# Kernel optimization log

Hardware: AMD Instinct MI355X
Metric: run time of the kernel (lower is better)

Reference implementation:

```python
import jax, jax.numpy as jnp
import numpy as np

N, E, B, D, H, L = 50000, 800000, 16, 64, 128, 2


def _lin(h, w, b):
    return h @ w + b


def _scatter_mean(v, idx, n):
    s = jax.ops.segment_sum(v, idx, num_segments=n)
    c = jax.ops.segment_sum(jnp.ones((v.shape[0],), v.dtype), idx, num_segments=n)
    return s / jnp.maximum(c, 1.0)[:, None]


def setup_inputs() -> dict:
    key = jax.random.key(0)
    ks = iter(jax.random.split(key, 40))

    def p(*shape):
        return jax.random.normal(next(ks), shape, dtype=jnp.float32) * 0.05

    inp = {
        "x": jax.random.normal(next(ks), (N, D), dtype=jnp.float32),
        "edge_attr": jax.random.normal(next(ks), (E, D), dtype=jnp.float32),
        "u": jax.random.normal(next(ks), (B, D), dtype=jnp.float32),
        "e_w1": p(L, 4 * D, H), "e_b1": p(L, H),
        "e_w2": p(L, H, H), "e_b2": p(L, H),
        "e_w3": p(L, H, D), "e_b3": p(L, D),
        "n1_w1": p(L, 2 * D, H), "n1_b1": p(L, H),
        "n1_w2": p(L, H, H), "n1_b2": p(L, H),
        "n2_w1": p(L, D + H + D, H), "n2_b1": p(L, H),
        "n2_w2": p(L, H, D), "n2_b2": p(L, D),
        "g_w1": p(L, 3 * D, H), "g_b1": p(L, H),
        "g_w2": p(L, H, D), "g_b2": p(L, D),
        "edge_index": jax.random.randint(next(ks), (2, E), 0, N, dtype=jnp.int32),
        "batch": jnp.sort(jax.random.randint(next(ks), (N,), 0, B, dtype=jnp.int32)),
    }
    return inp


def _forward(x, edge_attr, u, params, edge_index, batch):
    row, col = edge_index[0], edge_index[1]
    eb = batch[row]  # [E] graph id per edge
    x0, e0, u0 = x, edge_attr, u
    for l in range(L):
        (e_w1, e_b1, e_w2, e_b2, e_w3, e_b3,
         n1_w1, n1_b1, n1_w2, n1_b2,
         n2_w1, n2_b1, n2_w2, n2_b2,
         g_w1, g_b1, g_w2, g_b2) = [pm[l] for pm in params]
        # Edge model: [E, e+2n+u] -> MLP -> [E, D]
        h = jnp.concatenate([x[row], x[col], edge_attr, u[eb]], axis=1)
        h = jax.nn.relu(_lin(h, e_w1, e_b1))
        h = jax.nn.relu(_lin(h, e_w2, e_b2))
        edge_attr = _lin(h, e_w3, e_b3)
        # Node model: gather src node + edge, MLP1, scatter_mean onto dest, MLP2
        se = jnp.concatenate([x[row], edge_attr], axis=1)  # [E, 2D]
        se = _lin(jax.nn.relu(_lin(se, n1_w1, n1_b1)), n1_w2, n1_b2)
        agg = _scatter_mean(se, col, N)  # [N, H]
        xh = jnp.concatenate([x, agg, u[batch]], axis=1)
        x = _lin(jax.nn.relu(_lin(xh, n2_w1, n2_b1)), n2_w2, n2_b2)
        # Global model: per-graph means of updated nodes/edges
        e_agg = _scatter_mean(edge_attr, eb, B)
        n_agg = _scatter_mean(x, batch, B)
        uh = jnp.concatenate([u, n_agg, e_agg], axis=1)
        u = _lin(jax.nn.relu(_lin(uh, g_w1, g_b1)), g_w2, g_b2)
    return x + x0, edge_attr + e0, u + u0


def reference(x, edge_attr, u, e_w1, e_b1, e_w2, e_b2, e_w3, e_b3, n1_w1, n1_b1, n1_w2, n1_b2, n2_w1, n2_b1, n2_w2, n2_b2, g_w1, g_b1, g_w2, g_b2, edge_index, batch):
    params = (e_w1, e_b1, e_w2, e_b2, e_w3, e_b3,
              n1_w1, n1_b1, n1_w2, n1_b2,
              n2_w1, n2_b1, n2_w2, n2_b2,
              g_w1, g_b1, g_w2, g_b2)
    return _forward(x, edge_attr, u, params, edge_index, batch)
```

## Files before the change

kernel.cpp:

```cpp
#include <hip/hip_runtime.h>

#define N_NODES 50000
#define E_EDGES 800000
#define NG 16
#define DD 64
#define HH 128
#define NB_SCAN 49
#define EREP 32

typedef __attribute__((ext_vector_type(8))) __bf16 bf16x8;
typedef __attribute__((ext_vector_type(4))) float f32x4;
typedef unsigned int uint;
typedef unsigned short ushort;
typedef __attribute__((ext_vector_type(4))) uint uint4v;

#define MFMA16(a,b,c) __builtin_amdgcn_mfma_f32_16x16x32_bf16((a),(b),(c),0,0,0)

__device__ __forceinline__ ushort f2bf(float f){
  uint u = __builtin_bit_cast(uint, f);
  u += 0x7fffu + ((u >> 16) & 1u);
  return (ushort)(u >> 16);
}
__device__ __forceinline__ uint pk2(float a, float b){
  return (uint)f2bf(a) | ((uint)f2bf(b) << 16);
}
__device__ __forceinline__ float bflo(uint u){ return __builtin_bit_cast(float, u << 16); }
__device__ __forceinline__ float bfhi(uint u){ return __builtin_bit_cast(float, u & 0xffff0000u); }

__device__ __forceinline__ void bar(){
  asm volatile("s_waitcnt lgkmcnt(0)" ::: "memory");
  __builtin_amdgcn_s_barrier();
}
#define VMWAIT(n) asm volatile("s_waitcnt vmcnt(" #n ")" ::: "memory")

__device__ __forceinline__ void gload16(const void* g, void* l){
  __builtin_amdgcn_global_load_lds(
      (const __attribute__((address_space(1))) unsigned int*)g,
      (__attribute__((address_space(3))) unsigned int*)l, 16, 0, 0);
}

__device__ __forceinline__ bf16x8 ldfrag(const char* base, int row, int byteoff){
  uint4v v = *(const uint4v*)(base + row*256 + (byteoff ^ ((row & 7) << 4)));
  return __builtin_bit_cast(bf16x8, v);
}
__device__ __forceinline__ uint4v ld_chunk(const char* base, int row, int c16){
  return *(const uint4v*)(base + row*256 + ((c16*16) ^ ((row & 7) << 4)));
}
__device__ __forceinline__ void st_h(char* base, int row, int col, float v){
  *(ushort*)(base + row*256 + ((col*2) ^ ((row & 7) << 4))) = f2bf(v);
}
__device__ __forceinline__ void st_chunk(char* base, int row, int c16, uint4v v){
  *(uint4v*)(base + row*256 + ((c16*16) ^ ((row & 7) << 4))) = v;
}
__device__ __forceinline__ bf16x8 ldfrag128(const char* base, int row, int byteoff){
  uint4v v = *(const uint4v*)(base + row*128 + (byteoff ^ ((row & 7) << 4)));
  return __builtin_bit_cast(bf16x8, v);
}
__device__ __forceinline__ void st_chunk128(char* base, int row, int c16, uint4v v){
  *(uint4v*)(base + row*128 + ((c16*16) ^ ((row & 7) << 4))) = v;
}
__device__ __forceinline__ void pack16_128(char* dst, int r, int c16, const float* src){
  float4 lo = *(const float4*)src;
  float4 hi = *(const float4*)(src + 4);
  uint4v v; v.x = pk2(lo.x, lo.y); v.y = pk2(lo.z, lo.w);
  v.z = pk2(hi.x, hi.y); v.w = pk2(hi.z, hi.w);
  st_chunk128(dst, r, c16, v);
}

__device__ __forceinline__ void stage_b(char* sB, const ushort* wt,
                                        int Nout, int Ktot, int koff, int t, int stride){
  for (int task = t; task < Nout*16; task += stride){
    int n = task >> 4, c = task & 15;
    uint4v v = *(const uint4v*)(wt + (long)n*Ktot + koff + c*8);
    st_chunk(sB, n, c, v);
  }
}
template<int NT>
__device__ __forceinline__ void gemm_acc(const char* A, const char* B,
                                         int wv, int l15, int lhi, f32x4* acc){
  #pragma unroll
  for (int kt = 0; kt < 4; ++kt){
    bf16x8 a = ldfrag(A, wv*16 + l15, kt*64 + lhi*16);
    #pragma unroll
    for (int n = 0; n < NT; ++n){
      bf16x8 bb = ldfrag(B, n*16 + l15, kt*64 + lhi*16);
      acc[n] = MFMA16(a, bb, acc[n]);
    }
  }
}
template<int NT, bool RELU>
__device__ __forceinline__ void epi_lds(char* dst, const f32x4* acc, const float* bias,
                                        int wv, int l15, int lhi){
  #pragma unroll
  for (int n = 0; n < NT; ++n){
    float bv = bias[n*16 + l15];
    #pragma unroll
    for (int j = 0; j < 4; ++j){
      int r = wv*16 + lhi*4 + j;
      float v = acc[n][j] + bv;
      if (RELU) v = fmaxf(v, 0.f);
      st_h(dst, r, n*16 + l15, v);
    }
  }
}

__global__ void convert_x(const float* __restrict__ x, ushort* __restrict__ xbf){
  int i = blockIdx.x*256 + threadIdx.x;
  if (i < (N_NODES*DD)/8){
    float4 lo = *(const float4*)(x + (long)i*8);
    float4 hi = *(const float4*)(x + (long)i*8 + 4);
    uint4v v; v.x = pk2(lo.x, lo.y); v.y = pk2(lo.z, lo.w);
    v.z = pk2(hi.x, hi.y); v.w = pk2(hi.z, hi.w);
    *(uint4v*)(xbf + (long)i*8) = v;
  }
}

__global__ void pack_weights(const float* __restrict__ e1, const float* __restrict__ e2,
                             const float* __restrict__ e3, const float* __restrict__ n12,
                             const float* __restrict__ n21, const float* __restrict__ n22,
                             ushort* __restrict__ out){
  int idx = blockIdx.x * 256 + threadIdx.x;
  int l = idx / 114688, r = idx % 114688;
  const float* src; int K, N, off;
  if      (r <  32768){ src = e1;  K = 256; N = 128; off = 0; }
  else if (r <  49152){ src = e2;  K = 128; N = 128; off = 32768; }
  else if (r <  57344){ src = e3;  K = 128; N = 64;  off = 49152; }
  else if (r <  73728){ src = n12; K = 128; N = 128; off = 57344; }
  else if (r < 106496){ src = n21; K = 256; N = 128; off = 73728; }
  else                { src = n22; K = 128; N = 64;  off = 106496; }
  int q = r - off; int k = q / N; int n = q % N;
  out[(long)l*139264 + off + n*K + k] = f2bf(src[(long)l*K*N + q]);
}

__global__ void make_wc(const float* __restrict__ n1w1, const float* __restrict__ ew3,
                        const float* __restrict__ n1b1, const float* __restrict__ eb3,
                        ushort* __restrict__ packed, float* __restrict__ biasc){
  int l = blockIdx.x, t = threadIdx.x;
  const float* W1 = n1w1 + (long)l*128*128;
  const float* W3 = ew3 + (long)l*128*64;
  ushort* wc = packed + (long)l*139264 + 114688;
  for (int i = t; i < 8192; i += 256){
    int k = i >> 7, n = i & 127;
    wc[n*192 + k] = f2bf(W1[k*128 + n]);
  }
  for (int i = t; i < 16384; i += 256){
    int k2 = i >> 7, n = i & 127;
    float s = 0.f;
    for (int m = 0; m < 64; ++m) s += W3[k2*64 + m] * W1[(64 + m)*128 + n];
    wc[n*192 + 64 + k2] = f2bf(s);
  }
  if (t < 128){
    float s = n1b1[l*128 + t];
    for (int m = 0; m < 64; ++m) s += eb3[l*64 + m] * W1[(64 + m)*128 + t];
    biasc[l*128 + t] = s;
  }
}

__global__ void hist_kernel(const int* __restrict__ edge_index, const int* __restrict__ batch,
                            int* __restrict__ deg, float* __restrict__ cnt_eb){
  __shared__ float h[NG];
  int t = threadIdx.x;
  if (t < NG) h[t] = 0.f;
  __syncthreads();
  int e = blockIdx.x * 256 + t;
  if (e < E_EDGES){
    atomicAdd(deg + edge_index[E_EDGES + e], 1);
    atomicAdd(&h[batch[edge_index[e]]], 1.f);
  }
  __syncthreads();
  if (t < NG) atomicAdd(cnt_eb + t, h[t]);
}
__global__ void count_nodes_kernel(const int* __restrict__ batch, float* __restrict__ cnt_b){
  __shared__ float h[NG];
  int t = threadIdx.x;
  if (t < NG) h[t] = 0.f;
  __syncthreads();
  int n = blockIdx.x * 256 + t;
  if (n < N_NODES) atomicAdd(&h[batch[n]], 1.f);
  __syncthreads();
  if (t < NG) atomicAdd(cnt_b + t, h[t]);
}
__global__ void scan_a(const int* __restrict__ deg, int* __restrict__ bsum){
  __shared__ int red[1024];
  int i = blockIdx.x*1024 + threadIdx.x;
  red[threadIdx.x] = (i < N_NODES) ? deg[i] : 0;
  __syncthreads();
  for (int s = 512; s > 0; s >>= 1){
    if ((int)threadIdx.x < s) red[threadIdx.x] += red[threadIdx.x + s];
    __syncthreads();
  }
  if (threadIdx.x == 0) bsum[blockIdx.x] = red[0];
}
__global__ void scan_b(const int* __restrict__ bsum, int* __restrict__ bbase){
  if (threadIdx.x == 0){
    int run = 0;
    for (int b = 0; b < NB_SCAN; ++b){ int v = bsum[b]; bbase[b] = run; run += v; }
  }
}
__global__ void scan_c(const int* __restrict__ deg, const int* __restrict__ bbase,
                       int* __restrict__ off, int* __restrict__ cursor){
  __shared__ int sc[1024];
  int i = blockIdx.x*1024 + threadIdx.x;
  int v = (i < N_NODES) ? deg[i] : 0;
  sc[threadIdx.x] = v;
  __syncthreads();
  for (int d = 1; d < 1024; d <<= 1){
    int add = ((int)threadIdx.x >= d) ? sc[threadIdx.x - d] : 0;
    __syncthreads();
    sc[threadIdx.x] += add;
    __syncthreads();
  }
  if (i < N_NODES){
    int ex = sc[threadIdx.x] - v + bbase[blockIdx.x];
    off[i] = ex; cursor[i] = ex;
  }
}
__global__ void fill_kernel(const int* __restrict__ edge_index, int* __restrict__ cursor,
                            int* __restrict__ pos){
  int e = blockIdx.x*256 + threadIdx.x;
  if (e < E_EDGES){
    int c = edge_index[E_EDGES + e];
    pos[e] = atomicAdd(&cursor[c], 1);
  }
}

__global__ __launch_bounds__(256, 3) void k123_kernel(
    const ushort* __restrict__ xbf, const float* e_cur,
    const float* __restrict__ u_cur,
    const int* __restrict__ ei, const int* __restrict__ batch,
    const ushort* __restrict__ w1t, const ushort* __restrict__ w2t,
    const float* __restrict__ be1, const float* __restrict__ be2,
    ushort* h2g)
{
  __shared__ __align__(16) char lds[49152];
  __shared__ int sRow[128], sCol[128], sEb[128];
  char* A  = lds;
  char* B  = lds + 16384;
  char* OV = lds + 16384;
  const int t = threadIdx.x;
  const int wv = t >> 6, l15 = t & 15, lhi = (t >> 4) & 3;
  const int ebase = blockIdx.x * 128;

  if (t < 128){
    int r = ei[ebase + t];
    sRow[t] = r; sCol[t] = ei[E_EDGES + ebase + t]; sEb[t] = batch[r];
  }
  __syncthreads();

  f32x4 acc[2][8];
  #pragma unroll
  for (int m = 0; m < 2; ++m)
    #pragma unroll
    for (int n = 0; n < 8; ++n) acc[m][n] = f32x4{0,0,0,0};

  for (int c = 0; c < 4; ++c){
    #pragma unroll
    for (int it = 0; it < 4; ++it){
      int task = t + it*256, r = task >> 3, c16 = task & 7;
      if (c == 0)
        st_chunk128(A, r, c16, *(const uint4v*)(xbf + (long)sRow[r]*DD + c16*8));
      else if (c == 1)
        st_chunk128(A, r, c16, *(const uint4v*)(xbf + (long)sCol[r]*DD + c16*8));
      else if (c == 2)
        pack16_128(A, r, c16, e_cur + (long)(ebase + r)*DD + c16*8);
      else
        pack16_128(A, r, c16, u_cur + (long)sEb[r]*DD + c16*8);
    }
    #pragma unroll
    for (int it = 0; it < 4; ++it){
      int task = t + it*256, n = task >> 3, c16 = task & 7;
      st_chunk128(B, n, c16, *(const uint4v*)(w1t + (long)n*256 + c*64 + c16*8));
    }
    __syncthreads();
    #pragma unroll
    for (int kt = 0; kt < 2; ++kt){
      bf16x8 a0 = ldfrag128(A, wv*32 + l15,      kt*64 + lhi*16);
      bf16x8 a1 = ldfrag128(A, wv*32 + 16 + l15, kt*64 + lhi*16);
      #pragma unroll
      for (int n = 0; n < 8; ++n){
        bf16x8 bb = ldfrag128(B, n*16 + l15, kt*64 + lhi*16);
        acc[0][n] = MFMA16(a0, bb, acc[0][n]);
        acc[1][n] = MFMA16(a1, bb, acc[1][n]);
      }
    }
    __syncthreads();
  }
  #pragma unroll
  for (int m = 0; m < 2; ++m)
    #pragma unroll
    for (int n = 0; n < 8; ++n){
      int col = n*16 + l15;
      float bv = be1[col];
      #pragma unroll
      for (int j = 0; j < 4; ++j)
        st_h(OV, wv*32 + m*16 + lhi*4 + j, col, fmaxf(acc[m][n][j] + bv, 0.f));
    }
  __syncthreads();

  #pragma unroll
  for (int m = 0; m < 2; ++m)
    #pragma unroll
    for (int n = 0; n < 8; ++n) acc[m][n] = f32x4{0,0,0,0};
  for (int kc = 0; kc < 2; ++kc){
    #pragma unroll
    for (int it = 0; it < 4; ++it){
      int task = t + it*256, n = task >> 3, c16 = task & 7;
      st_chunk128(A, n, c16, *(const uint4v*)(w2t + (long)n*128 + kc*64 + c16*8));
    }
    __syncthreads();
    #pragma unroll
    for (int kt = 0; kt < 2; ++kt){
      bf16x8 a0 = ldfrag(OV, wv*32 + l15,      kc*128 + kt*64 + lhi*16);
      bf16x8 a1 = ldfrag(OV, wv*32 + 16 + l15, kc*128 + kt*64 + lhi*16);
      #pragma unroll
      for (int n = 0; n < 8; ++n){
        bf16x8 bb = ldfrag128(A, n*16 + l15, kt*64 + lhi*16);
        acc[0][n] = MFMA16(a0, bb, acc[0][n]);
        acc[1][n] = MFMA16(a1, bb, acc[1][n]);
      }
    }
    __syncthreads();
  }
  #pragma unroll
  for (int m = 0; m < 2; ++m)
    #pragma unroll
    for (int n = 0; n < 8; ++n){
      int col = n*16 + l15;
      float bv = be2[col];
      #pragma unroll
      for (int j = 0; j < 4; ++j)
        st_h(OV, wv*32 + m*16 + lhi*4 + j, col, fmaxf(acc[m][n][j] + bv, 0.f));
    }
  __syncthreads();
  #pragma unroll
  for (int it = 0; it < 8; ++it){
    int task = t + it*256, r = task >> 4, c16 = task & 15;
    *(uint4v*)(h2g + (long)(ebase + r)*HH + c16*8) = ld_chunk(OV, r, c16);
  }
}

template<bool CSR>
__global__ __launch_bounds__(256, 2) void k45_kernel(
    const ushort* __restrict__ xbf, const ushort* h2g,
    const int* __restrict__ ei, const int* __restrict__ batch,
    const int* __restrict__ pos_arr,
    const ushort* __restrict__ w3t, const ushort* __restrict__ wct,
    const ushort* __restrict__ w5t,
    const float* __restrict__ be3, const float* __restrict__ biasc,
    const float* __restrict__ bn12,
    float* e_outf, const float* __restrict__ e_resid,
    ushort* __restrict__ se_buf, float* __restrict__ agg_sum,
    float* __restrict__ e_agg_rep, int has_resid)
{
  __shared__ __align__(16) char lds[49152];
  __shared__ float sEagg[NG*DD];
  __shared__ int sRow[128];
  __shared__ int sDst[128];
  char* S0 = lds;
  char* S1 = lds + 16384;
  char* S2 = lds + 32768;
  char* OV = lds;
  const int t = threadIdx.x;
  const int wv = t >> 6, lane = t & 63, l15 = t & 15, lhi = (t >> 4) & 3;
  const int ebase = blockIdx.x * 128;

  auto GL = [&](const ushort* base, long stride, int koff, char* slot){
    #pragma unroll
    for (int it = 0; it < 4; ++it){
      int q = (wv*4 + it)*64 + lane;
      int r = q >> 3, cp = q & 7;
      gload16(base + (long)r*stride + koff + ((cp ^ (r & 7))*8),
              slot + (wv*4 + it)*1024);
    }
  };

  if (t < 128){
    int r = ei[ebase + t];
    sDst[t] = CSR ? pos_arr[ebase + t] : ei[E_EDGES + ebase + t];
    sRow[t] = r | (batch[r] << 16);
  }
  GL(wct, 192, 0, S1);
  GL(h2g + (long)ebase*HH, HH, 0, S2);
  bf16x8 b3[4][4];
  #pragma unroll
  for (int n = 0; n < 4; ++n)
    #pragma unroll
    for (int kk = 0; kk < 4; ++kk)
      b3[n][kk] = *(const bf16x8*)(w3t + (long)(n*16 + l15)*128 + kk*32 + lhi*8);
  for (int i = t; i < NG*DD; i += 256) sEagg[i] = 0.f;
  __syncthreads();

  #pragma unroll
  for (int it = 0; it < 4; ++it){
    int task = t + it*256, r = task >> 3, c16 = task & 7;
    st_chunk128(S0, r, c16,
        *(const uint4v*)(xbf + (long)(sRow[r] & 0xffff)*DD + c16*8));
  }
  __syncthreads();

  f32x4 acc4[2][8], acc3[2][4];
  #pragma unroll
  for (int m = 0; m < 2; ++m){
    #pragma unroll
    for (int n = 0; n < 8; ++n) acc4[m][n] = f32x4{0,0,0,0};
    #pragma unroll
    for (int n = 0; n < 4; ++n) acc3[m][n] = f32x4{0,0,0,0};
  }
  auto MM = [&](const char* A, const char* B){
    #pragma unroll
    for (int kt = 0; kt < 2; ++kt){
      bf16x8 a0 = ldfrag128(A, wv*32 + l15,      kt*64 + lhi*16);
      bf16x8 a1 = ldfrag128(A, wv*32 + 16 + l15, kt*64 + lhi*16);
      #pragma unroll
      for (int n = 0; n < 8; ++n){
        bf16x8 bb = ldfrag128(B, n*16 + l15, kt*64 + lhi*16);
        acc4[0][n] = MFMA16(a0, bb, acc4[0][n]);
        acc4[1][n] = MFMA16(a1, bb, acc4[1][n]);
      }
    }
  };
  auto MM3 = [&](const char* A, const char* B, int kkbase){
    #pragma unroll
    for (int kt = 0; kt < 2; ++kt){
      bf16x8 a0 = ldfrag128(A, wv*32 + l15,      kt*64 + lhi*16);
      bf16x8 a1 = ldfrag128(A, wv*32 + 16 + l15, kt*64 + lhi*16);
      #pragma unroll
      for (int n = 0; n < 8; ++n){
        bf16x8 bb = ldfrag128(B, n*16 + l15, kt*64 + lhi*16);
        acc4[0][n] = MFMA16(a0, bb, acc4[0][n]);
        acc4[1][n] = MFMA16(a1, bb, acc4[1][n]);
      }
      #pragma unroll
      for (int n = 0; n < 4; ++n){
        acc3[0][n] = MFMA16(a0, b3[n][kkbase + kt], acc3[0][n]);
        acc3[1][n] = MFMA16(a1, b3[n][kkbase + kt], acc3[1][n]);
      }
    }
  };

  MM(S0, S1);
  bar();
  GL(wct, 192, 64, S1);
  GL(h2g + (long)ebase*HH, HH, 64, S0);
  VMWAIT(4);
  __builtin_amdgcn_s_barrier();
  MM3(S2, S1, 0);
  bar();
  GL(wct, 192, 128, S1);
  GL(w5t, 128, 0, S2);
  VMWAIT(4);
  __builtin_amdgcn_s_barrier();
  MM3(S0, S1, 2);
  bar();
  #pragma unroll
  for (int m = 0; m < 2; ++m)
    #pragma unroll
    for (int n = 0; n < 8; ++n){
      int col = n*16 + l15;
      float bv = biasc[col];
      #pragma unroll
      for (int j = 0; j < 4; ++j)
        st_h(OV, wv*32 + m*16 + lhi*4 + j, col, fmaxf(acc4[m][n][j] + bv, 0.f));
    }
  VMWAIT(0);
  bar();
  f32x4 acc5[2][8];
  #pragma unroll
  for (int m = 0; m < 2; ++m)
    #pragma unroll
    for (int n = 0; n < 8; ++n) acc5[m][n] = f32x4{0,0,0,0};
  #pragma unroll
  for (int kt = 0; kt < 2; ++kt){
    bf16x8 a0 = ldfrag(OV, wv*32 + l15,      kt*64 + lhi*16);
    bf16x8 a1 = ldfrag(OV, wv*32 + 16 + l15, kt*64 + lhi*16);
    #pragma unroll
    for (int n = 0; n < 8; ++n){
      bf16x8 bb = ldfrag128(S2, n*16 + l15, kt*64 + lhi*16);
      acc5[0][n] = MFMA16(a0, bb, acc5[0][n]);
      acc5[1][n] = MFMA16(a1, bb, acc5[1][n]);
    }
  }
  bar();
  GL(w5t, 128, 64, S2);
  VMWAIT(0);
  __builtin_amdgcn_s_barrier();
  #pragma unroll
  for (int kt = 0; kt < 2; ++kt){
    bf16x8 a0 = ldfrag(OV, wv*32 + l15,      128 + kt*64 + lhi*16);
    bf16x8 a1 = ldfrag(OV, wv*32 + 16 + l15, 128 + kt*64 + lhi*16);
    #pragma unroll
    for (int n = 0; n < 8; ++n){
      bf16x8 bb = ldfrag128(S2, n*16 + l15, kt*64 + lhi*16);
      acc5[0][n] = MFMA16(a0, bb, acc5[0][n]);
      acc5[1][n] = MFMA16(a1, bb, acc5[1][n]);
    }
  }
  bar();

  if (CSR){
    #pragma unroll
    for (int m = 0; m < 2; ++m)
      #pragma unroll
      for (int n = 0; n < 8; ++n){
        int col = n*16 + l15;
        float bv = bn12[col];
        #pragma unroll
        for (int j = 0; j < 4; ++j)
          st_h(OV, wv*32 + m*16 + lhi*4 + j, col, acc5[m][n][j] + bv);
      }
    bar();
    #pragma unroll
    for (int it = 0; it < 8; ++it){
      int task = t + it*256, r = task >> 4, c16 = task & 15;
      *(uint4v*)(se_buf + (long)sDst[r]*HH + c16*8) = ld_chunk(OV, r, c16);
    }
  } else {
    #pragma unroll
    for (int m = 0; m < 2; ++m)
      #pragma unroll
      for (int n = 0; n < 8; ++n){
        int col = n*16 + l15;
        float bv = bn12[col];
        #pragma unroll
        for (int j = 0; j < 4; ++j){
          int row = wv*32 + m*16 + lhi*4 + j;
          atomicAdd(agg_sum + (long)sDst[row]*HH + col, acc5[m][n][j] + bv);
        }
      }
  }
  #pragma unroll
  for (int m = 0; m < 2; ++m)
    #pragma unroll
    for (int n = 0; n < 4; ++n){
      int col = n*16 + l15;
      float bv = be3[col];
      #pragma unroll
      for (int j = 0; j < 4; ++j){
        int row = wv*32 + m*16 + lhi*4 + j;
        float v = acc3[m][n][j] + bv;
        long eg = (long)(ebase + row)*DD + col;
        e_outf[eg] = has_resid ? (v + e_resid[eg]) : v;
        atomicAdd(&sEagg[(sRow[row] >> 16)*DD + col], v);
      }
    }
  __syncthreads();
  float* dst = e_agg_rep + (long)(blockIdx.x & (EREP - 1))*NG*DD;
  for (int i = t; i < NG*DD; i += 256) atomicAdd(dst + i, sEagg[i]);
}

template<bool CSR>
__global__ __launch_bounds__(256, 2) void node_kernel(
    const float* __restrict__ x_cur, const float* __restrict__ u_cur,
    const float* __restrict__ x_resid, const int* __restrict__ batch,
    const ushort* __restrict__ se_buf, const int* __restrict__ deg,
    const int* __restrict__ off, const float* __restrict__ agg_sum,
    const ushort* __restrict__ w_n21, const ushort* __restrict__ w_n22,
    const float* __restrict__ b_n21, const float* __restrict__ b_n22,
    float* __restrict__ x_out, float* __restrict__ n_agg, int has_resid)
{
  __shared__ __align__(16) char sA[16384];
  __shared__ __align__(16) char sB[32768];
  __shared__ __align__(16) char sH[16384];
  __shared__ int sBat[64], sDeg[64], sOff[64];
  __shared__ float sRinv[64];
  __shared__ float sNagg[NG*DD];

  const int t = threadIdx.x;
  const int wv = t >> 6, ln = t & 63, l15 = ln & 15, lhi = ln >> 4;
  const int n0 = blockIdx.x * 64;

  if (t < 64){
    int nd = n0 + t;
    int ok = nd < N_NODES;
    sBat[t] = ok ? batch[nd] : 0;
    int d = ok ? deg[nd] : 0;
    sDeg[t] = d;
    sOff[t] = ok ? off[nd] : 0;
    sRinv[t] = 1.f / fmaxf((float)d, 1.f);
  }
  for (int i = t; i < NG*DD; i += 256) sNagg[i] = 0.f;
  __syncthreads();

  float s[32];
  const int r4 = t >> 2, q = t & 3;
  if (CSR){
    #pragma unroll
    for (int k = 0; k < 32; ++k) s[k] = 0.f;
    int d = sDeg[r4], o = sOff[r4];
    for (int i = 0; i < d; ++i){
      const ushort* src = se_buf + (long)(o + i)*HH + q*32;
      #pragma unroll
      for (int c = 0; c < 4; ++c){
        uint4v v = *(const uint4v*)(src + c*8);
        #pragma unroll
        for (int jj = 0; jj < 4; ++jj){
          s[c*8 + jj*2]     += bflo(v[jj]);
          s[c*8 + jj*2 + 1] += bfhi(v[jj]);
        }
      }
    }
    float riv = sRinv[r4];
    #pragma unroll
    for (int k = 0; k < 32; ++k) s[k] *= riv;
  }

  f32x4 acc[8];
  #pragma unroll
  for (int n = 0; n < 8; ++n) acc[n] = f32x4{0.f,0.f,0.f,0.f};

  for (int half = 0; half < 2; ++half){
    if (CSR){
      for (int task = t; task < 512; task += 256){
        int r = task >> 3, c = task & 7;
        int nd = n0 + r;
        bool ok = nd < N_NODES;
        float4 lo = {0,0,0,0}, hi = {0,0,0,0};
        if (ok){
          const float* src = (half == 0) ? (x_cur + (long)nd*DD + c*8)
                                         : (u_cur + (long)sBat[r]*DD + c*8);
          lo = *(const float4*)src; hi = *(const float4*)(src + 4);
        }
        uint4v v; v.x = pk2(lo.x, lo.y); v.y = pk2(lo.z, lo.w);
        v.z = pk2(hi.x, hi.y); v.w = pk2(hi.z, hi.w);
        st_chunk(sA, r, (half == 0) ? c : (8 + c), v);
      }
      if ((half == 0 && q < 2) || (half == 1 && q >= 2)){
        int cbase = (half == 0) ? (8 + q*4) : ((q - 2)*4);
        #pragma unroll
        for (int cc = 0; cc < 4; ++cc){
          uint4v v;
          v.x = pk2(s[cc*8+0], s[cc*8+1]); v.y = pk2(s[cc*8+2], s[cc*8+3]);
          v.z = pk2(s[cc*8+4], s[cc*8+5]); v.w = pk2(s[cc*8+6], s[cc*8+7]);
          st_chunk(sA, r4, cbase + cc, v);
        }
      }
    } else {
      for (int task = t; task < 1024; task += 256){
        int r = task >> 4, c = task & 15;
        int nd = n0 + r;
        bool ok = nd < N_NODES;
        float scale = 1.f;
        const float* src;
        if (half == 0){
          if (c < 8) src = x_cur + (long)nd*DD + c*8;
          else { src = agg_sum + (long)nd*HH + (c-8)*8; scale = sRinv[r]; }
        } else {
          if (c < 8){ src = agg_sum + (long)nd*HH + 64 + c*8; scale = sRinv[r]; }
          else src = u_cur + (long)sBat[r]*DD + (c-8)*8;
        }
        float4 lo = {0,0,0,0}, hi = {0,0,0,0};
        if (ok){ lo = *(const float4*)src; hi = *(const float4*)(src + 4); }
        uint4v v; v.x = pk2(lo.x*scale, lo.y*scale); v.y = pk2(lo.z*scale, lo.w*scale);
        v.z = pk2(hi.x*scale, hi.y*scale); v.w = pk2(hi.z*scale, hi.w*scale);
        st_chunk(sA, r, c, v);
      }
    }
    stage_b(sB, w_n21, 128, 256, half*128, t, 256);
    __syncthreads();
    gemm_acc<8>(sA, sB, wv, l15, lhi, acc);
    __syncthreads();
  }
  epi_lds<8, true>(sH, acc, b_n21, wv, l15, lhi);
  stage_b(sB, w_n22, 64, 128, 0, t, 256);
  __syncthreads();

  f32x4 acc2[4];
  #pragma unroll
  for (int n = 0; n < 4; ++n) acc2[n] = f32x4{0.f,0.f,0.f,0.f};
  gemm_acc<4>(sH, sB, wv, l15, lhi, acc2);

  #pragma unroll
  for (int n = 0; n < 4; ++n){
    float bv = b_n22[n*16 + l15];
    #pragma unroll
    for (int j = 0; j < 4; ++j){
      int r = wv*16 + lhi*4 + j;
      int nd = n0 + r;
      if (nd < N_NODES){
        int col = n*16 + l15;
        float v = acc2[n][j] + bv;
        long xg = (long)nd*DD + col;
        x_out[xg] = has_resid ? (v + x_resid[xg]) : v;
        atomicAdd(&sNagg[sBat[r]*DD + col], v);
      }
    }
  }
  __syncthreads();
  for (int i = t; i < NG*DD; i += 256) atomicAdd(n_agg + i, sNagg[i]);
}

__global__ void global_kernel(const float* __restrict__ u_cur, const float* __restrict__ n_agg,
                              const float* __restrict__ e_agg_rep, const float* __restrict__ cnt_b,
                              const float* __restrict__ cnt_e,
                              const float* __restrict__ g_w1, const float* __restrict__ g_b1,
                              const float* __restrict__ g_w2, const float* __restrict__ g_b2,
                              const float* __restrict__ u_resid, float* __restrict__ u_out,
                              int has_resid)
{
  int g = blockIdx.x, t = threadIdx.x;
  __shared__ float uh[192];
  __shared__ float hb[128];
  float v;
  if (t < 64)       v = u_cur[g*64 + t];
  else if (t < 128) v = n_agg[g*64 + (t-64)] / fmaxf(cnt_b[g], 1.f);
  else {
    float s = 0.f;
    for (int c = 0; c < EREP; ++c) s += e_agg_rep[c*NG*DD + g*64 + (t-128)];
    v = s / fmaxf(cnt_e[g], 1.f);
  }
  uh[t] = v;
  __syncthreads();
  if (t < 128){
    float s = g_b1[t];
    for (int k = 0; k < 192; ++k) s += uh[k] * g_w1[k*128 + t];
    hb[t] = fmaxf(s, 0.f);
  }
  __syncthreads();
  if (t < 64){
    float s = g_b2[t];
    for (int k = 0; k < 128; ++k) s += hb[k] * g_w2[k*64 + t];
    if (has_resid) s += u_resid[g*64 + t];
    u_out[g*64 + t] = s;
  }
}

extern "C" void kernel_launch(void* const* d_in, const int* in_sizes, int n_in,
                              void* d_out, int out_size, void* d_ws, size_t ws_size,
                              hipStream_t stream)
{
  const float* x0   = (const float*)d_in[0];
  const float* e0   = (const float*)d_in[1];
  const float* u0   = (const float*)d_in[2];
  const float* e_w1 = (const float*)d_in[3];
  const float* e_b1 = (const float*)d_in[4];
  const float* e_w2 = (const float*)d_in[5];
  const float* e_b2 = (const float*)d_in[6];
  const float* e_w3 = (const float*)d_in[7];
  const float* e_b3 = (const float*)d_in[8];
  const float* n1_w1 = (const float*)d_in[9];
  const float* n1_b1 = (const float*)d_in[10];
  const float* n1_w2 = (const float*)d_in[11];
  const float* n1_b2 = (const float*)d_in[12];
  const float* n2_w1 = (const float*)d_in[13];
  const float* n2_b1 = (const float*)d_in[14];
  const float* n2_w2 = (const float*)d_in[15];
  const float* n2_b2 = (const float*)d_in[16];
  const float* g_w1 = (const float*)d_in[17];
  const float* g_b1 = (const float*)d_in[18];
  const float* g_w2 = (const float*)d_in[19];
  const float* g_b2 = (const float*)d_in[20];
  const int* edge_index = (const int*)d_in[21];
  const int* batch      = (const int*)d_in[22];

  float* out_x = (float*)d_out;
  float* out_e = out_x + (long)N_NODES*DD;
  float* out_u = out_e + (long)E_EDGES*DD;

  char* ws = (char*)d_ws;
  int*   deg    = (int*)(ws + 0);
  int*   off    = (int*)(ws + 200000);
  int*   cursor = (int*)(ws + 400000);
  int*   bsum   = (int*)(ws + 600000);
  int*   bbase  = (int*)(ws + 600256);
  float* cnt_eb = (float*)(ws + 600512);
  float* cnt_b  = (float*)(ws + 600576);
  float* n_agg  = (float*)(ws + 604736);
  float* biascf = (float*)(ws + 608832);
  ushort* packed = (ushort*)(ws + 609856);
  float* e_agg_rep = (float*)(ws + 1166912);
  ushort* xbf = (ushort*)(ws + 1297984);
  const size_t big = 7697984;
  bool use_csr = ws_size >= (size_t)(big + 204800000 + 3200000);
  ushort* se_buf = (ushort*)(ws + big);
  int*    pos    = (int*)(ws + big + 204800000);
  float*  agg_sum = (float*)(ws + big);

  (void)hipMemsetAsync(deg, 0, 200000, stream);
  (void)hipMemsetAsync(cnt_eb, 0, 128, stream);
  pack_weights<<<896, 256, 0, stream>>>(e_w1, e_w2, e_w3, n1_w2, n2_w1, n2_w2, packed);
  make_wc<<<2, 256, 0, stream>>>(n1_w1, e_w3, n1_b1, e_b3, packed, biascf);
  hist_kernel<<<3125, 256, 0, stream>>>(edge_index, batch, deg, cnt_eb);
  count_nodes_kernel<<<196, 256, 0, stream>>>(batch, cnt_b);
  if (use_csr){
    scan_a<<<NB_SCAN, 1024, 0, stream>>>(deg, bsum);
    scan_b<<<1, 64, 0, stream>>>(bsum, bbase);
    scan_c<<<NB_SCAN, 1024, 0, stream>>>(deg, bbase, off, cursor);
    fill_kernel<<<3125, 256, 0, stream>>>(edge_index, cursor, pos);
  }

  const float* xc = x0;
  const float* ec = e0;
  const float* uc = u0;
  for (int l = 0; l < 2; ++l){
    (void)hipMemsetAsync(n_agg, 0, 4096, stream);
    (void)hipMemsetAsync(e_agg_rep, 0, EREP*NG*DD*4, stream);
    if (!use_csr)
      (void)hipMemsetAsync(agg_sum, 0, (size_t)N_NODES*HH*4, stream);
    convert_x<<<1563, 256, 0, stream>>>(xc, xbf);
    const ushort* P = packed + (long)l*139264;
    k123_kernel<<<6250, 256, 0, stream>>>(
        xbf, ec, uc, edge_index, batch,
        P + 0, P + 32768, e_b1 + l*128, e_b2 + l*128,
        (ushort*)out_e);
    if (use_csr){
      k45_kernel<true><<<6250, 256, 0, stream>>>(
          xbf, (const ushort*)out_e, edge_index, batch, pos,
          P + 49152, P + 114688, P + 57344,
          e_b3 + l*64, biascf + l*128, n1_b2 + l*128,
          out_e, e0, se_buf, agg_sum, e_agg_rep, l == 1);
      node_kernel<true><<<782, 256, 0, stream>>>(
          xc, uc, x0, batch, se_buf, deg, off, agg_sum,
          P + 73728, P + 106496, n2_b1 + l*128, n2_b2 + l*64,
          out_x, n_agg, l == 1);
    } else {
      k45_kernel<false><<<6250, 256, 0, stream>>>(
          xbf, (const ushort*)out_e, edge_index, batch, pos,
          P + 49152, P + 114688, P + 57344,
          e_b3 + l*64, biascf + l*128, n1_b2 + l*128,
          out_e, e0, se_buf, agg_sum, e_agg_rep, l == 1);
      node_kernel<false><<<782, 256, 0, stream>>>(
          xc, uc, x0, batch, se_buf, deg, off, agg_sum,
          P + 73728, P + 106496, n2_b1 + l*128, n2_b2 + l*64,
          out_x, n_agg, l == 1);
    }
    global_kernel<<<NG, 192, 0, stream>>>(
        uc, n_agg, e_agg_rep, cnt_b, cnt_eb,
        g_w1 + l*192*128, g_b1 + l*128, g_w2 + l*128*64, g_b2 + l*64,
        u0, out_u, l == 1);
    xc = out_x; ec = out_e; uc = out_u;
  }
}
```

Baseline: 1.758 ms.

## Fuse edge MLP and node-MLP1 into one kernel with 64-edge tiles

Merges the separate edge-MLP (k123) and node-message (k45) kernels into a single edge_fused kernel that processes 64 edges per block. The intermediate h2 no longer makes a round trip through global memory, and weights are staged through double-buffered LDS slots. Layer-0 edge output is written as bf16 for the layer-1 read, and node_kernel emits bf16 x directly so the per-layer convert_x launch is removed on the CSR path. The trade-offs are more LDS per block (about 72KB), lower occupancy, and re-staging all weights for every 64-edge tile. The async global_load_lds path is also replaced with plain synchronous loads.

```diff
diff --git a/kernel.cpp b/kernel.cpp
--- a/kernel.cpp
+++ b/kernel.cpp
@@ -31,13 +31,6 @@
   asm volatile("s_waitcnt lgkmcnt(0)" ::: "memory");
   __builtin_amdgcn_s_barrier();
 }
-#define VMWAIT(n) asm volatile("s_waitcnt vmcnt(" #n ")" ::: "memory")
-
-__device__ __forceinline__ void gload16(const void* g, void* l){
-  __builtin_amdgcn_global_load_lds(
-      (const __attribute__((address_space(1))) unsigned int*)g,
-      (__attribute__((address_space(3))) unsigned int*)l, 16, 0, 0);
-}
 
 __device__ __forceinline__ bf16x8 ldfrag(const char* base, int row, int byteoff){
   uint4v v = *(const uint4v*)(base + row*256 + (byteoff ^ ((row & 7) << 4)));
@@ -56,8 +49,14 @@
   uint4v v = *(const uint4v*)(base + row*128 + (byteoff ^ ((row & 7) << 4)));
   return __builtin_bit_cast(bf16x8, v);
 }
+__device__ __forceinline__ uint4v ld_chunk128(const char* base, int row, int c16){
+  return *(const uint4v*)(base + row*128 + ((c16*16) ^ ((row & 7) << 4)));
+}
 __device__ __forceinline__ void st_chunk128(char* base, int row, int c16, uint4v v){
   *(uint4v*)(base + row*128 + ((c16*16) ^ ((row & 7) << 4))) = v;
+}
+__device__ __forceinline__ void st_h128(char* base, int row, int col, float v){
+  *(ushort*)(base + row*128 + ((col*2) ^ ((row & 7) << 4))) = f2bf(v);
 }
 __device__ __forceinline__ void pack16_128(char* dst, int r, int c16, const float* src){
   float4 lo = *(const float4*)src;
@@ -224,163 +223,54 @@
   }
 }
 
-__global__ __launch_bounds__(256, 3) void k123_kernel(
-    const ushort* __restrict__ xbf, const float* e_cur,
+template<bool CSR, bool EBF>
+__global__ __launch_bounds__(256, 2) void edge_fused(
+    const ushort* __restrict__ xbf, const float* e_f32, const ushort* e_bf,
     const float* __restrict__ u_cur,
     const int* __restrict__ ei, const int* __restrict__ batch,
+    const int* __restrict__ pos_arr,
     const ushort* __restrict__ w1t, const ushort* __restrict__ w2t,
-    const float* __restrict__ be1, const float* __restrict__ be2,
-    ushort* h2g)
-{
-  __shared__ __align__(16) char lds[49152];
-  __shared__ int sRow[128], sCol[128], sEb[128];
-  char* A  = lds;
-  char* B  = lds + 16384;
-  char* OV = lds + 16384;
-  const int t = threadIdx.x;
-  const int wv = t >> 6, l15 = t & 15, lhi = (t >> 4) & 3;
-  const int ebase = blockIdx.x * 128;
-
-  if (t < 128){
-    int r = ei[ebase + t];
-    sRow[t] = r; sCol[t] = ei[E_EDGES + ebase + t]; sEb[t] = batch[r];
-  }
-  __syncthreads();
-
-  f32x4 acc[2][8];
-  #pragma unroll
-  for (int m = 0; m < 2; ++m)
-    #pragma unroll
-    for (int n = 0; n < 8; ++n) acc[m][n] = f32x4{0,0,0,0};
-
-  for (int c = 0; c < 4; ++c){
-    #pragma unroll
-    for (int it = 0; it < 4; ++it){
-      int task = t + it*256, r = task >> 3, c16 = task & 7;
-      if (c == 0)
-        st_chunk128(A, r, c16, *(const uint4v*)(xbf + (long)sRow[r]*DD + c16*8));
-      else if (c == 1)
-        st_chunk128(A, r, c16, *(const uint4v*)(xbf + (long)sCol[r]*DD + c16*8));
-      else if (c == 2)
-        pack16_128(A, r, c16, e_cur + (long)(ebase + r)*DD + c16*8);
-      else
-        pack16_128(A, r, c16, u_cur + (long)sEb[r]*DD + c16*8);
-    }
-    #pragma unroll
-    for (int it = 0; it < 4; ++it){
-      int task = t + it*256, n = task >> 3, c16 = task & 7;
-      st_chunk128(B, n, c16, *(const uint4v*)(w1t + (long)n*256 + c*64 + c16*8));
-    }
-    __syncthreads();
-    #pragma unroll
-    for (int kt = 0; kt < 2; ++kt){
-      bf16x8 a0 = ldfrag128(A, wv*32 + l15,      kt*64 + lhi*16);
-      bf16x8 a1 = ldfrag128(A, wv*32 + 16 + l15, kt*64 + lhi*16);
-      #pragma unroll
-      for (int n = 0; n < 8; ++n){
-        bf16x8 bb = ldfrag128(B, n*16 + l15, kt*64 + lhi*16);
-        acc[0][n] = MFMA16(a0, bb, acc[0][n]);
-        acc[1][n] = MFMA16(a1, bb, acc[1][n]);
-      }
-    }
-    __syncthreads();
-  }
-  #pragma unroll
-  for (int m = 0; m < 2; ++m)
-    #pragma unroll
-    for (int n = 0; n < 8; ++n){
-      int col = n*16 + l15;
-      float bv = be1[col];
-      #pragma unroll
-      for (int j = 0; j < 4; ++j)
-        st_h(OV, wv*32 + m*16 + lhi*4 + j, col, fmaxf(acc[m][n][j] + bv, 0.f));
-    }
-  __syncthreads();
-
-  #pragma unroll
-  for (int m = 0; m < 2; ++m)
-    #pragma unroll
-    for (int n = 0; n < 8; ++n) acc[m][n] = f32x4{0,0,0,0};
-  for (int kc = 0; kc < 2; ++kc){
-    #pragma unroll
-    for (int it = 0; it < 4; ++it){
-      int task = t + it*256, n = task >> 3, c16 = task & 7;
-      st_chunk128(A, n, c16, *(const uint4v*)(w2t + (long)n*128 + kc*64 + c16*8));
-    }
-    __syncthreads();
-    #pragma unroll
-    for (int kt = 0; kt < 2; ++kt){
-      bf16x8 a0 = ldfrag(OV, wv*32 + l15,      kc*128 + kt*64 + lhi*16);
-      bf16x8 a1 = ldfrag(OV, wv*32 + 16 + l15, kc*128 + kt*64 + lhi*16);
-      #pragma unroll
-      for (int n = 0; n < 8; ++n){
-        bf16x8 bb = ldfrag128(A, n*16 + l15, kt*64 + lhi*16);
-        acc[0][n] = MFMA16(a0, bb, acc[0][n]);
-        acc[1][n] = MFMA16(a1, bb, acc[1][n]);
-      }
-    }
-    __syncthreads();
-  }
-  #pragma unroll
-  for (int m = 0; m < 2; ++m)
-    #pragma unroll
-    for (int n = 0; n < 8; ++n){
-      int col = n*16 + l15;
-      float bv = be2[col];
-      #pragma unroll
-      for (int j = 0; j < 4; ++j)
-        st_h(OV, wv*32 + m*16 + lhi*4 + j, col, fmaxf(acc[m][n][j] + bv, 0.f));
-    }
-  __syncthreads();
-  #pragma unroll
-  for (int it = 0; it < 8; ++it){
-    int task = t + it*256, r = task >> 4, c16 = task & 15;
-    *(uint4v*)(h2g + (long)(ebase + r)*HH + c16*8) = ld_chunk(OV, r, c16);
-  }
-}
-
-template<bool CSR>
-__global__ __launch_bounds__(256, 2) void k45_kernel(
-    const ushort* __restrict__ xbf, const ushort* h2g,
-    const int* __restrict__ ei, const int* __restrict__ batch,
-    const int* __restrict__ pos_arr,
     const ushort* __restrict__ w3t, const ushort* __restrict__ wct,
     const ushort* __restrict__ w5t,
+    const float* __restrict__ be1, const float* __restrict__ be2,
     const float* __restrict__ be3, const float* __restrict__ biasc,
     const float* __restrict__ bn12,
     float* e_outf, const float* __restrict__ e_resid,
     ushort* __restrict__ se_buf, float* __restrict__ agg_sum,
     float* __restrict__ e_agg_rep, int has_resid)
 {
-  __shared__ __align__(16) char lds[49152];
+  __shared__ __align__(16) char lds[73728];
   __shared__ float sEagg[NG*DD];
-  __shared__ int sRow[128];
-  __shared__ int sDst[128];
-  char* S0 = lds;
-  char* S1 = lds + 16384;
-  char* S2 = lds + 32768;
-  char* OV = lds;
+  __shared__ int sRow[64];
+  __shared__ int sCol[64];
+  __shared__ int sDst[64];
+  char* X  = lds;
+  char* A0 = lds + 8192;
+  char* A1 = lds + 16384;
+  char* W0 = lds + 24576;
+  char* W1 = lds + 40960;
+  char* OV = lds + 57344;
   const int t = threadIdx.x;
-  const int wv = t >> 6, lane = t & 63, l15 = t & 15, lhi = (t >> 4) & 3;
-  const int ebase = blockIdx.x * 128;
-
-  auto GL = [&](const ushort* base, long stride, int koff, char* slot){
+  const int wv = t >> 6, l15 = t & 15, lhi = (t >> 4) & 3;
+  const int ebase = blockIdx.x * 64;
+
+  auto WSTAGE = [&](char* W, const ushort* wt, int K, int coff){
     #pragma unroll
     for (int it = 0; it < 4; ++it){
-      int q = (wv*4 + it)*64 + lane;
-      int r = q >> 3, cp = q & 7;
-      gload16(base + (long)r*stride + koff + ((cp ^ (r & 7))*8),
-              slot + (wv*4 + it)*1024);
+      int task = t + it*256, n = task >> 3, c16 = task & 7;
+      st_chunk128(W, n, c16, *(const uint4v*)(wt + (long)n*K + coff + c16*8));
     }
   };
 
-  if (t < 128){
+  if (t < 64){
     int r = ei[ebase + t];
-    sDst[t] = CSR ? pos_arr[ebase + t] : ei[E_EDGES + ebase + t];
+    int c = ei[E_EDGES + ebase + t];
     sRow[t] = r | (batch[r] << 16);
-  }
-  GL(wct, 192, 0, S1);
-  GL(h2g + (long)ebase*HH, HH, 0, S2);
+    sCol[t] = c;
+    sDst[t] = CSR ? pos_arr[ebase + t] : c;
+  }
+  WSTAGE(W0, w1t, 256, 0);
+  WSTAGE(W1, w1t, 256, 64);
   bf16x8 b3[4][4];
   #pragma unroll
   for (int n = 0; n < 4; ++n)
@@ -390,159 +280,220 @@
   for (int i = t; i < NG*DD; i += 256) sEagg[i] = 0.f;
   __syncthreads();
 
-  #pragma unroll
-  for (int it = 0; it < 4; ++it){
+  uint4v xr[2], xc[2], eu[2];
+  float4 ef[4];
+  #pragma unroll
+  for (int it = 0; it < 2; ++it){
     int task = t + it*256, r = task >> 3, c16 = task & 7;
-    st_chunk128(S0, r, c16,
-        *(const uint4v*)(xbf + (long)(sRow[r] & 0xffff)*DD + c16*8));
-  }
-  __syncthreads();
-
-  f32x4 acc4[2][8], acc3[2][4];
-  #pragma unroll
-  for (int m = 0; m < 2; ++m){
-    #pragma unroll
-    for (int n = 0; n < 8; ++n) acc4[m][n] = f32x4{0,0,0,0};
-    #pragma unroll
-    for (int n = 0; n < 4; ++n) acc3[m][n] = f32x4{0,0,0,0};
-  }
-  auto MM = [&](const char* A, const char* B){
+    xr[it] = *(const uint4v*)(xbf + (long)(sRow[r] & 0xffff)*DD + c16*8);
+    xc[it] = *(const uint4v*)(xbf + (long)sCol[r]*DD + c16*8);
+    if (EBF) eu[it] = *(const uint4v*)(e_bf + (long)(ebase + r)*HH + c16*8);
+    else { ef[2*it]   = *(const float4*)(e_f32 + (long)(ebase + r)*DD + c16*8);
+           ef[2*it+1] = *(const float4*)(e_f32 + (long)(ebase + r)*DD + c16*8 + 4); }
+  }
+  #pragma unroll
+  for (int it = 0; it < 2; ++it){
+    int task = t + it*256, r = task >> 3, c16 = task & 7;
+    st_chunk128(X, r, c16, xr[it]);
+  }
+  __syncthreads();
+
+  f32x4 acc1[8];
+  #pragma unroll
+  for (int n = 0; n < 8; ++n) acc1[n] = f32x4{0,0,0,0};
+  auto MM128 = [&](const char* A, const char* W, f32x4* acc){
     #pragma unroll
     for (int kt = 0; kt < 2; ++kt){
-      bf16x8 a0 = ldfrag128(A, wv*32 + l15,      kt*64 + lhi*16);
-      bf16x8 a1 = ldfrag128(A, wv*32 + 16 + l15, kt*64 + lhi*16);
+      bf16x8 a = ldfrag128(A, wv*16 + l15, kt*64 + lhi*16);
       #pragma unroll
       for (int n = 0; n < 8; ++n){
-        bf16x8 bb = ldfrag128(B, n*16 + l15, kt*64 + lhi*16);
-        acc4[0][n] = MFMA16(a0, bb, acc4[0][n]);
-        acc4[1][n] = MFMA16(a1, bb, acc4[1][n]);
+        bf16x8 bb = ldfrag128(W, n*16 + l15, kt*64 + lhi*16);
+        acc[n] = MFMA16(a, bb, acc[n]);
       }
     }
   };
-  auto MM3 = [&](const char* A, const char* B, int kkbase){
+  f32x4 acc3[4];
+  #pragma unroll
+  for (int n = 0; n < 4; ++n) acc3[n] = f32x4{0,0,0,0};
+  auto MMOV = [&](int cbase, const char* W, f32x4* acc){
     #pragma unroll
     for (int kt = 0; kt < 2; ++kt){
-      bf16x8 a0 = ldfrag128(A, wv*32 + l15,      kt*64 + lhi*16);
-      bf16x8 a1 = ldfrag128(A, wv*32 + 16 + l15, kt*64 + lhi*16);
+      bf16x8 a = ldfrag(OV, wv*16 + l15, cbase + kt*64 + lhi*16);
       #pragma unroll
       for (int n = 0; n < 8; ++n){
-        bf16x8 bb = ldfrag128(B, n*16 + l15, kt*64 + lhi*16);
-        acc4[0][n] = MFMA16(a0, bb, acc4[0][n]);
-        acc4[1][n] = MFMA16(a1, bb, acc4[1][n]);
-      }
-      #pragma unroll
-      for (int n = 0; n < 4; ++n){
-        acc3[0][n] = MFMA16(a0, b3[n][kkbase + kt], acc3[0][n]);
-        acc3[1][n] = MFMA16(a1, b3[n][kkbase + kt], acc3[1][n]);
+        bf16x8 bb = ldfrag128(W, n*16 + l15, kt*64 + lhi*16);
+        acc[n] = MFMA16(a, bb, acc[n]);
       }
     }
   };
-
-  MM(S0, S1);
-  bar();
-  GL(wct, 192, 64, S1);
-  GL(h2g + (long)ebase*HH, HH, 64, S0);
-  VMWAIT(4);
-  __builtin_amdgcn_s_barrier();
-  MM3(S2, S1, 0);
-  bar();
-  GL(wct, 192, 128, S1);
-  GL(w5t, 128, 0, S2);
-  VMWAIT(4);
-  __builtin_amdgcn_s_barrier();
-  MM3(S0, S1, 2);
-  bar();
-  #pragma unroll
-  for (int m = 0; m < 2; ++m)
+  auto MMOV3 = [&](int cbase, const char* W, f32x4* acc, int kkb){
+    #pragma unroll
+    for (int kt = 0; kt < 2; ++kt){
+      bf16x8 a = ldfrag(OV, wv*16 + l15, cbase + kt*64 + lhi*16);
+      #pragma unroll
+      for (int n = 0; n < 8; ++n){
+        bf16x8 bb = ldfrag128(W, n*16 + l15, kt*64 + lhi*16);
+        acc[n] = MFMA16(a, bb, acc[n]);
+      }
+      #pragma unroll
+      for (int n = 0; n < 4; ++n)
+        acc3[n] = MFMA16(a, b3[n][kkb + kt], acc3[n]);
+    }
+  };
+  auto EPI = [&](const float* bias, const f32x4* acc, bool relu){
     #pragma unroll
     for (int n = 0; n < 8; ++n){
       int col = n*16 + l15;
-      float bv = biasc[col];
+      float bv = bias[col];
+      #pragma unroll
+      for (int j = 0; j < 4; ++j){
+        float v = acc[n][j] + bv;
+        if (relu) v = fmaxf(v, 0.f);
+        st_h(OV, wv*16 + lhi*4 + j, col, v);
+      }
+    }
+  };
+
+  MM128(X, W0, acc1);
+  #pragma unroll
+  for (int it = 0; it < 2; ++it){
+    int task = t + it*256, r = task >> 3, c16 = task & 7;
+    st_chunk128(A0, r, c16, xc[it]);
+  }
+  bar();
+  MM128(A0, W1, acc1);
+  WSTAGE(W0, w1t, 256, 128);
+  #pragma unroll
+  for (int it = 0; it < 2; ++it){
+    int task = t + it*256, r = task >> 3, c16 = task & 7;
+    if (EBF) st_chunk128(A1, r, c16, eu[it]);
+    else {
+      uint4v v; v.x = pk2(ef[2*it].x, ef[2*it].y);     v.y = pk2(ef[2*it].z, ef[2*it].w);
+      v.z = pk2(ef[2*it+1].x, ef[2*it+1].y); v.w = pk2(ef[2*it+1].z, ef[2*it+1].w);
+      st_chunk128(A1, r, c16, v);
+    }
+  }
+  bar();
+  MM128(A1, W0, acc1);
+  WSTAGE(W1, w1t, 256, 192);
+  #pragma unroll
+  for (int it = 0; it < 2; ++it){
+    int task = t + it*256, r = task >> 3, c16 = task & 7;
+    pack16_128(A0, r, c16, u_cur + (long)(sRow[r] >> 16)*DD + c16*8);
+  }
+  bar();
+  MM128(A0, W1, acc1);
+  WSTAGE(W0, w2t, 128, 0);
+  EPI(be1, acc1, true);
+  bar();
+  f32x4 acc2[8];
+  #pragma unroll
+  for (int n = 0; n < 8; ++n) acc2[n] = f32x4{0,0,0,0};
+  MMOV(0, W0, acc2);
+  WSTAGE(W1, w2t, 128, 64);
+  bar();
+  MMOV(128, W1, acc2);
+  WSTAGE(W0, wct, 192, 0);
+  EPI(be2, acc2, true);
+  bar();
+  f32x4 acc4[8];
+  #pragma unroll
+  for (int n = 0; n < 8; ++n) acc4[n] = f32x4{0,0,0,0};
+  MM128(X, W0, acc4);
+  WSTAGE(W1, wct, 192, 64);
+  bar();
+  MMOV3(0, W1, acc4, 0);
+  WSTAGE(W0, wct, 192, 128);
+  bar();
+  MMOV3(128, W0, acc4, 2);
+  WSTAGE(W1, w5t, 128, 0);
+  EPI(biasc, acc4, true);
+  bar();
+  f32x4 acc5[8];
+  #pragma unroll
+  for (int n = 0; n < 8; ++n) acc5[n] = f32x4{0,0,0,0};
+  MMOV(0, W1, acc5);
+  WSTAGE(W0, w5t, 128, 64);
+  bar();
+  MMOV(128, W0, acc5);
+  bar();
+
+  if (CSR){
+    #pragma unroll
+    for (int n = 0; n < 8; ++n){
+      int col = n*16 + l15;
+      float bv = bn12[col];
       #pragma unroll
       for (int j = 0; j < 4; ++j)
-        st_h(OV, wv*32 + m*16 + lhi*4 + j, col, fmaxf(acc4[m][n][j] + bv, 0.f));
-    }
-  VMWAIT(0);
-  bar();
-  f32x4 acc5[2][8];
-  #pragma unroll
-  for (int m = 0; m < 2; ++m)
-    #pragma unroll
-    for (int n = 0; n < 8; ++n) acc5[m][n] = f32x4{0,0,0,0};
-  #pragma unroll
-  for (int kt = 0; kt < 2; ++kt){
-    bf16x8 a0 = ldfrag(OV, wv*32 + l15,      kt*64 + lhi*16);
-    bf16x8 a1 = ldfrag(OV, wv*32 + 16 + l15, kt*64 + lhi*16);
-    #pragma unroll
-    for (int n = 0; n < 8; ++n){
-      bf16x8 bb = ldfrag128(S2, n*16 + l15, kt*64 + lhi*16);
-      acc5[0][n] = MFMA16(a0, bb, acc5[0][n]);
-      acc5[1][n] = MFMA16(a1, bb, acc5[1][n]);
-    }
-  }
-  bar();
-  GL(w5t, 128, 64, S2);
-  VMWAIT(0);
-  __builtin_amdgcn_s_barrier();
-  #pragma unroll
-  for (int kt = 0; kt < 2; ++kt){
-    bf16x8 a0 = ldfrag(OV, wv*32 + l15,      128 + kt*64 + lhi*16);
-    bf16x8 a1 = ldfrag(OV, wv*32 + 16 + l15, 128 + kt*64 + lhi*16);
-    #pragma unroll
-    for (int n = 0; n < 8; ++n){
-      bf16x8 bb = ldfrag128(S2, n*16 + l15, kt*64 + lhi*16);
-      acc5[0][n] = MFMA16(a0, bb, acc5[0][n]);
-      acc5[1][n] = MFMA16(a1, bb, acc5[1][n]);
-    }
-  }
-  bar();
-
-  if (CSR){
-    #pragma unroll
-    for (int m = 0; m < 2; ++m)
-      #pragma unroll
-      for (int n = 0; n < 8; ++n){
+        st_h(OV, wv*16 + lhi*4 + j, col, acc5[n][j] + bv);
+    }
+    if (!has_resid){
+      #pragma unroll
+      for (int n = 0; n < 4; ++n){
         int col = n*16 + l15;
-        float bv = bn12[col];
+        float bv = be3[col];
         #pragma unroll
-        for (int j = 0; j < 4; ++j)
-          st_h(OV, wv*32 + m*16 + lhi*4 + j, col, acc5[m][n][j] + bv);
-      }
+        for (int j = 0; j < 4; ++j){
+          int row = wv*16 + lhi*4 + j;
+          float v = acc3[n][j] + bv;
+          st_h128(A0, row, col, v);
+          atomicAdd(&sEagg[(sRow[row] >> 16)*DD + col], v);
+        }
+      }
+    } else {
+      #pragma unroll
+      for (int n = 0; n < 4; ++n){
+        int col = n*16 + l15;
+        float bv = be3[col];
+        #pragma unroll
+        for (int j = 0; j < 4; ++j){
+          int row = wv*16 + lhi*4 + j;
+          float v = acc3[n][j] + bv;
+          long eg = (long)(ebase + row)*DD + col;
+          e_outf[eg] = v + e_resid[eg];
+          atomicAdd(&sEagg[(sRow[row] >> 16)*DD + col], v);
+        }
+      }
+    }
     bar();
     #pragma unroll
-    for (int it = 0; it < 8; ++it){
+    for (int it = 0; it < 4; ++it){
       int task = t + it*256, r = task >> 4, c16 = task & 15;
       *(uint4v*)(se_buf + (long)sDst[r]*HH + c16*8) = ld_chunk(OV, r, c16);
     }
+    if (!has_resid){
+      ushort* ebf_out = (ushort*)e_outf;
+      #pragma unroll
+      for (int it = 0; it < 2; ++it){
+        int task = t + it*256, r = task >> 3, c16 = task & 7;
+        *(uint4v*)(ebf_out + (long)(ebase + r)*HH + c16*8) = ld_chunk128(A0, r, c16);
+      }
+    }
   } else {
     #pragma unroll
-    for (int m = 0; m < 2; ++m)
-      #pragma unroll
-      for (int n = 0; n < 8; ++n){
-        int col = n*16 + l15;
-        float bv = bn12[col];
-        #pragma unroll
-        for (int j = 0; j < 4; ++j){
-          int row = wv*32 + m*16 + lhi*4 + j;
-          atomicAdd(agg_sum + (long)sDst[row]*HH + col, acc5[m][n][j] + bv);
-        }
-      }
-  }
-  #pragma unroll
-  for (int m = 0; m < 2; ++m)
+    for (int n = 0; n < 8; ++n){
+      int col = n*16 + l15;
+      float bv = bn12[col];
+      #pragma unroll
+      for (int j = 0; j < 4; ++j){
+        int row = wv*16 + lhi*4 + j;
+        atomicAdd(agg_sum + (long)sDst[row]*HH + col, acc5[n][j] + bv);
+      }
+    }
     #pragma unroll
     for (int n = 0; n < 4; ++n){
       int col = n*16 + l15;
       float bv = be3[col];
       #pragma unroll
       for (int j = 0; j < 4; ++j){
-        int row = wv*32 + m*16 + lhi*4 + j;
-        float v = acc3[m][n][j] + bv;
+        int row = wv*16 + lhi*4 + j;
+        float v = acc3[n][j] + bv;
         long eg = (long)(ebase + row)*DD + col;
         e_outf[eg] = has_resid ? (v + e_resid[eg]) : v;
         atomicAdd(&sEagg[(sRow[row] >> 16)*DD + col], v);
       }
     }
+  }
   __syncthreads();
   float* dst = e_agg_rep + (long)(blockIdx.x & (EREP - 1))*NG*DD;
   for (int i = t; i < NG*DD; i += 256) atomicAdd(dst + i, sEagg[i]);
@@ -556,7 +507,8 @@
     const int* __restrict__ off, const float* __restrict__ agg_sum,
     const ushort* __restrict__ w_n21, const ushort* __restrict__ w_n22,
     const float* __restrict__ b_n21, const float* __restrict__ b_n22,
-    float* __restrict__ x_out, float* __restrict__ n_agg, int has_resid)
+    float* __restrict__ x_out, ushort* __restrict__ xbf_out,
+    float* __restrict__ n_agg, int has_resid)
 {
   __shared__ __align__(16) char sA[16384];
   __shared__ __align__(16) char sB[32768];
@@ -680,7 +632,9 @@
         int col = n*16 + l15;
         float v = acc2[n][j] + bv;
         long xg = (long)nd*DD + col;
-        x_out[xg] = has_resid ? (v + x_resid[xg]) : v;
+        float vw = has_resid ? (v + x_resid[xg]) : v;
+        x_out[xg] = vw;
+        if (!has_resid) xbf_out[xg] = f2bf(vw);
         atomicAdd(&sNagg[sBat[r]*DD + col], v);
       }
     }
@@ -781,6 +735,7 @@
   make_wc<<<2, 256, 0, stream>>>(n1_w1, e_w3, n1_b1, e_b3, packed, biascf);
   hist_kernel<<<3125, 256, 0, stream>>>(edge_index, batch, deg, cnt_eb);
   count_nodes_kernel<<<196, 256, 0, stream>>>(batch, cnt_b);
+  convert_x<<<1563, 256, 0, stream>>>(x0, xbf);
   if (use_csr){
     scan_a<<<NB_SCAN, 1024, 0, stream>>>(deg, bsum);
     scan_b<<<1, 64, 0, stream>>>(bsum, bbase);
@@ -789,44 +744,48 @@
   }
 
   const float* xc = x0;
-  const float* ec = e0;
   const float* uc = u0;
   for (int l = 0; l < 2; ++l){
     (void)hipMemsetAsync(n_agg, 0, 4096, stream);
     (void)hipMemsetAsync(e_agg_rep, 0, EREP*NG*DD*4, stream);
-    if (!use_csr)
+    if (!use_csr){
       (void)hipMemsetAsync(agg_sum, 0, (size_t)N_NODES*HH*4, stream);
-    convert_x<<<1563, 256, 0, stream>>>(xc, xbf);
+      if (l == 1) convert_x<<<1563, 256, 0, stream>>>(xc, xbf);
+    }
     const ushort* P = packed + (long)l*139264;
-    k123_kernel<<<6250, 256, 0, stream>>>(
-        xbf, ec, uc, edge_index, batch,
-        P + 0, P + 32768, e_b1 + l*128, e_b2 + l*128,
-        (ushort*)out_e);
+    const float* ef32 = (l == 0) ? e0 : out_e;
     if (use_csr){
-      k45_kernel<true><<<6250, 256, 0, stream>>>(
-          xbf, (const ushort*)out_e, edge_index, batch, pos,
-          P + 49152, P + 114688, P + 57344,
-          e_b3 + l*64, biascf + l*128, n1_b2 + l*128,
-          out_e, e0, se_buf, agg_sum, e_agg_rep, l == 1);
+      if (l == 0)
+        edge_fused<true, false><<<12500, 256, 0, stream>>>(
+            xbf, e0, (const ushort*)out_e, uc, edge_index, batch, pos,
+            P + 0, P + 32768, P + 49152, P + 114688, P + 57344,
+            e_b1, e_b2, e_b3, biascf, n1_b2,
+            out_e, e0, se_buf, agg_sum, e_agg_rep, 0);
+      else
+        edge_fused<true, true><<<12500, 256, 0, stream>>>(
+            xbf, ef32, (const ushort*)out_e, uc, edge_index, batch, pos,
+            P + 0, P + 32768, P + 49152, P + 114688, P + 57344,
+            e_b1 + 128, e_b2 + 128, e_b3 + 64, biascf + 128, n1_b2 + 128,
+            out_e, e0, se_buf, agg_sum, e_agg_rep, 1);
       node_kernel<true><<<782, 256, 0, stream>>>(
           xc, uc, x0, batch, se_buf, deg, off, agg_sum,
           P + 73728, P + 106496, n2_b1 + l*128, n2_b2 + l*64,
-          out_x, n_agg, l == 1);
+          out_x, xbf, n_agg, l == 1);
     } else {
-      k45_kernel<false><<<6250, 256, 0, stream>>>(
-          xbf, (const ushort*)out_e, edge_index, batch, pos,
-          P + 49152, P + 114688, P + 57344,
-          e_b3 + l*64, biascf + l*128, n1_b2 + l*128,
+      edge_fused<false, false><<<12500, 256, 0, stream>>>(
+          xbf, ef32, (const ushort*)out_e, uc, edge_index, batch, pos,
+          P + 0, P + 32768, P + 49152, P + 114688, P + 57344,
+          e_b1 + l*128, e_b2 + l*128, e_b3 + l*64, biascf + l*128, n1_b2 + l*128,
           out_e, e0, se_buf, agg_sum, e_agg_rep, l == 1);
       node_kernel<false><<<782, 256, 0, stream>>>(
           xc, uc, x0, batch, se_buf, deg, off, agg_sum,
           P + 73728, P + 106496, n2_b1 + l*128, n2_b2 + l*64,
-          out_x, n_agg, l == 1);
+          out_x, xbf, n_agg, l == 1);
     }
     global_kernel<<<NG, 192, 0, stream>>>(
         uc, n_agg, e_agg_rep, cnt_b, cnt_eb,
         g_w1 + l*192*128, g_b1 + l*128, g_w2 + l*128*64, g_b2 + l*64,
         u0, out_u, l == 1);
-    xc = out_x; ec = out_e; uc = out_u;
-  }
-}
+    xc = out_x; uc = out_u;
+  }
+}
```

After: 1.767 ms. About the same (+0.6%).
